# Kernel optimization log

Measured on AMD Instinct MI355X. Metric: run time of the kernel, lower is better.

## Reference

```python
import jax, jax.numpy as jnp
import numpy as np

N = 50000
E = 800000
D = 128


def _gcn_layer(x, row, col, ew, W, b, n):
    # PyG GCNConv (normalize=True, add_self_loops=True):
    # self-loops were already appended to row/col/ew by the caller.
    deg = jax.ops.segment_sum(ew, col, num_segments=n)          # [N]
    dis = jnp.where(deg > 0, jax.lax.rsqrt(jnp.maximum(deg, 1e-12)), 0.0)
    norm = dis[row] * ew * dis[col]                              # [E+N]
    h = x @ W                                                    # [N, D]
    msg = h[row] * norm[:, None]                                 # [E+N, D] gather-scale
    out = jax.ops.segment_sum(msg, col, num_segments=n)          # scatter-add
    return out + b


def setup_inputs() -> dict:
    key = jax.random.key(0)
    k1, k2, k3, k4, k5 = jax.random.split(key, 5)
    x = jax.random.normal(k1, (N, D), dtype=jnp.float32)
    edge_index = jax.random.randint(k2, (2, E), 0, N, dtype=jnp.int64)
    edge_weight = jax.random.uniform(k3, (E,), dtype=jnp.float32)
    s = 1.0 / np.sqrt(D)
    W1 = jax.random.uniform(k4, (D, D), minval=-s, maxval=s, dtype=jnp.float32)
    b1 = jnp.zeros((D,), dtype=jnp.float32)
    W2 = jax.random.uniform(k5, (D, D), minval=-s, maxval=s, dtype=jnp.float32)
    b2 = jnp.zeros((D,), dtype=jnp.float32)
    return {"x": x, "edge_index": edge_index, "edge_weight": edge_weight,
            "W1": W1, "b1": b1, "W2": W2, "b2": b2}


def reference(x, edge_index, edge_weight, W1, b1, W2, b2):
    n = x.shape[0]
    loop = jnp.arange(n, dtype=edge_index.dtype)
    row = jnp.concatenate([edge_index[0], loop])
    col = jnp.concatenate([edge_index[1], loop])
    ew = jnp.concatenate([edge_weight, jnp.ones((n,), dtype=edge_weight.dtype)])
    h = _gcn_layer(x, row, col, ew, W1, b1, n)
    h = jax.nn.relu(h)
    # F.dropout(training=self.training): identity in eval mode
    out = _gcn_layer(h, row, col, ew, W2, b2, n)
    return out
```

## Files before the change

### kernel.cpp

```cpp
#include <hip/hip_runtime.h>

#define NN 50000
#define NE 800000
#define DD 128

#define FIX_SCALE 16777216.0f
#define LOW40 ((1ULL << 40) - 1)
#define NWELEM 16384
#define GEMM_GRID ((NN + 127) / 128)

#define SHIFT2 7
#define BWID 128
#define NBUCK ((NN + BWID - 1) / BWID)
#define CAP2 2560
#define NB1 500
#define EPB (NE / NB1)
#define EQ4 (EPB / 4)
#define NBK_PAD 392
#define HCAP 1536

typedef __attribute__((ext_vector_type(8))) short short8;
typedef __attribute__((ext_vector_type(4))) float floatx4;
typedef __attribute__((ext_vector_type(2))) _Float16 half2v;
typedef __attribute__((ext_vector_type(8))) _Float16 half8;


__device__ __forceinline__ void split_trunc(float x, short& hi, short& lo) {
    unsigned uh = __float_as_uint(x) >> 16;
    hi = (short)uh;
    float r = x - __uint_as_float(uh << 16);
    lo = (short)(__float_as_uint(r) >> 16);
}


__global__ __launch_bounds__(256) void init_hist(const int* __restrict__ col,
                                                 unsigned* __restrict__ hist,
                                                 const float* __restrict__ W1, const float* __restrict__ W2,
                                                 unsigned short* __restrict__ w1hi, unsigned short* __restrict__ w1lo,
                                                 unsigned short* __restrict__ w2hi, unsigned short* __restrict__ w2lo) {
    if (blockIdx.x < NB1) {
        __shared__ unsigned h[NBUCK];
        for (int k = threadIdx.x; k < NBUCK; k += 256) h[k] = 0u;
        __syncthreads();
        const int4* c4p = (const int4*)(col + blockIdx.x * EPB);
#pragma unroll
        for (int it = 0; it < 2; it++) {
            int q = it * 256 + (int)threadIdx.x;
            if (q < EQ4) {
                int4 c4 = c4p[q];
                atomicAdd(&h[c4.x >> SHIFT2], 1u);
                atomicAdd(&h[c4.y >> SHIFT2], 1u);
                atomicAdd(&h[c4.z >> SHIFT2], 1u);
                atomicAdd(&h[c4.w >> SHIFT2], 1u);
            }
        }
        __syncthreads();
        unsigned* hb = hist + (size_t)blockIdx.x * NBK_PAD;
        for (int k = threadIdx.x; k < NBUCK; k += 256) hb[k] = h[k];
    } else {
        int u = (blockIdx.x - NB1) * 256 + threadIdx.x;
        int which = u >> 14;
        int idx = u & (NWELEM - 1);
        int k = idx >> 7, n = idx & 127;
        const float* W = which ? W2 : W1;
        unsigned short* whi = which ? w2hi : w1hi;
        unsigned short* wlo = which ? w2lo : w1lo;
        short h, l;
        split_trunc(W[idx], h, l);
        whi[n * DD + k] = (unsigned short)h;
        wlo[n * DD + k] = (unsigned short)l;
    }
}


__global__ __launch_bounds__(512) void bucket_prefix(const unsigned* __restrict__ hist,
                                                     unsigned* __restrict__ offs_t,
                                                     unsigned* __restrict__ bcur) {
    __shared__ unsigned sa[512], sb[512];
    int k = blockIdx.x;
    int t = threadIdx.x;
    unsigned v = (t < NB1) ? hist[(size_t)t * NBK_PAD + k] : 0u;
    sa[t] = v;
    __syncthreads();
    unsigned* src = sa;
    unsigned* dst = sb;
    for (int d = 1; d < 512; d <<= 1) {
        unsigned x = src[t] + (t >= d ? src[t - d] : 0u);
        dst[t] = x;
        __syncthreads();
        unsigned* tmp = src; src = dst; dst = tmp;
    }
    unsigned inc = src[t];
    if (t < NB1) offs_t[(size_t)t * NBK_PAD + k] = inc - v;
    if (t == 511) bcur[k] = inc;
}


template <bool RELU, bool SCALE, typename InT>
__device__ __forceinline__ void gemm_core(int bid, const InT* __restrict__ in,
                                          const unsigned short* __restrict__ whi,
                                          const unsigned short* __restrict__ wlo,
                                          const float* __restrict__ dis,
                                          _Float16* __restrict__ out) {
    int lane = threadIdx.x & 63;
    int wid = threadIdx.x >> 6;
    int cg = wid & 1;
    int rg = wid >> 1;
    int l16 = lane & 15;
    int quad = lane >> 4;
    int koff_base = quad * 8;

    short8 bhi[4][4], blo[4][4];
#pragma unroll
    for (int t = 0; t < 4; t++) {
        int n = cg * 64 + t * 16 + l16;
#pragma unroll
        for (int ks = 0; ks < 4; ks++) {
            int koff = ks * 32 + koff_base;
            bhi[t][ks] = *(const short8*)(whi + n * DD + koff);
            blo[t][ks] = *(const short8*)(wlo + n * DD + koff);
        }
    }

#pragma unroll
    for (int chunk = 0; chunk < 4; chunk++) {
        int base = bid * 128 + chunk * 32 + rg * 16;
        int m = base + l16;
        int mld = (m < NN) ? m : 0;
        const InT* xr = in + (size_t)mld * DD;

        short8 ahi[4], alo[4];
#pragma unroll
        for (int ks = 0; ks < 4; ks++) {
            int koff = ks * 32 + koff_base;
            float v[8];
            if constexpr (sizeof(InT) == 4) {
                float4 a0 = *(const float4*)(xr + koff);
                float4 a1 = *(const float4*)(xr + koff + 4);
                v[0] = a0.x; v[1] = a0.y; v[2] = a0.z; v[3] = a0.w;
                v[4] = a1.x; v[5] = a1.y; v[6] = a1.z; v[7] = a1.w;
            } else {
                half8 a = *(const half8*)(xr + koff);
#pragma unroll
                for (int j = 0; j < 8; j++) v[j] = (float)a[j];
            }
#pragma unroll
            for (int j = 0; j < 8; j++) {
                float xv = RELU ? fmaxf(v[j], 0.0f) : v[j];
                short h, l;
                split_trunc(xv, h, l);
                ahi[ks][j] = h;
                alo[ks][j] = l;
            }
        }

        floatx4 acc[4];
#pragma unroll
        for (int t = 0; t < 4; t++) acc[t] = (floatx4)(0.0f);

#pragma unroll
        for (int ks = 0; ks < 4; ks++) {
#pragma unroll
            for (int t = 0; t < 4; t++) {
                acc[t] = __builtin_amdgcn_mfma_f32_16x16x32_bf16(ahi[ks], bhi[t][ks], acc[t], 0, 0, 0);
                acc[t] = __builtin_amdgcn_mfma_f32_16x16x32_bf16(alo[ks], bhi[t][ks], acc[t], 0, 0, 0);
                acc[t] = __builtin_amdgcn_mfma_f32_16x16x32_bf16(ahi[ks], blo[t][ks], acc[t], 0, 0, 0);
            }
        }

#pragma unroll
        for (int r = 0; r < 4; r++) {
            int rowm = base + quad * 4 + r;
            if (rowm < NN) {
                float dsc = SCALE ? dis[rowm] : 1.0f;
                _Float16* o = out + (size_t)rowm * DD + cg * 64 + l16;
#pragma unroll
                for (int t = 0; t < 4; t++) o[t * 16] = (_Float16)(acc[t][r] * dsc);
            }
        }
    }
}


__device__ __forceinline__ void scatter_core(int bid, const int* __restrict__ row,
                                             const int* __restrict__ col,
                                             const float* __restrict__ ew,
                                             const unsigned* __restrict__ offs_t,
                                             uint2* __restrict__ staged) {
    __shared__ unsigned base1[NBUCK];
    __shared__ unsigned cnt1[NBUCK];

    const unsigned* ob = offs_t + (size_t)bid * NBK_PAD;
    for (int k = threadIdx.x; k < NBUCK; k += 256) {
        base1[k] = (unsigned)k * CAP2 + ob[k];
        cnt1[k] = 0u;
    }
    __syncthreads();

    int e0 = bid * EPB;
    const int4* c4p = (const int4*)(col + e0);
    const int4* r4p = (const int4*)(row + e0);
    const float4* w4p = (const float4*)(ew + e0);

#pragma unroll
    for (int it = 0; it < 2; it++) {
        int q = it * 256 + (int)threadIdx.x;
        if (q < EQ4) {
            int4 c4 = c4p[q];
            int4 r4 = r4p[q];
            float4 w4 = w4p[q];
            int cc[4] = {c4.x, c4.y, c4.z, c4.w};
            int rr[4] = {r4.x, r4.y, r4.z, r4.w};
            float wv[4] = {w4.x, w4.y, w4.z, w4.w};
#pragma unroll
            for (int j = 0; j < 4; j++) {
                int bk = cc[j] >> SHIFT2;
                unsigned r = base1[bk] + atomicAdd(&cnt1[bk], 1u);
                unsigned lim = (unsigned)bk * CAP2 + (CAP2 - 1);
                if (r > lim) r = lim;
                uint2 p;
                p.x = (unsigned)rr[j] | ((unsigned)(cc[j] & (BWID - 1)) << 16);
                p.y = __float_as_uint(wv[j]);
                staged[r] = p;
            }
        }
    }
}


__global__ __launch_bounds__(256) void gemm1_scatter(const float* __restrict__ x,
                                                     const unsigned short* __restrict__ w1hi,
                                                     const unsigned short* __restrict__ w1lo,
                                                     _Float16* __restrict__ g,
                                                     const int* __restrict__ row,
                                                     const int* __restrict__ col,
                                                     const float* __restrict__ ew,
                                                     const unsigned* __restrict__ offs_t,
                                                     uint2* __restrict__ staged) {
    if (blockIdx.x < NB1) {
        scatter_core(blockIdx.x, row, col, ew, offs_t, staged);
    } else {
        gemm_core<false, false, float>(blockIdx.x - NB1, x, w1hi, w1lo, nullptr, g);
    }
}

__global__ __launch_bounds__(256, 2) void gemm2(const _Float16* __restrict__ in,
                                                const unsigned short* __restrict__ whi,
                                                const unsigned short* __restrict__ wlo,
                                                const float* __restrict__ dis,
                                                _Float16* __restrict__ out) {
    gemm_core<true, true, _Float16>(blockIdx.x, in, whi, wlo, dis, out);
}


__global__ __launch_bounds__(512) void bucket_sortdis(const unsigned* __restrict__ bcur,
                                                      const uint2* __restrict__ staged,
                                                      uint2* __restrict__ sorted,
                                                      unsigned* __restrict__ offcnt,
                                                      float* __restrict__ dis,
                                                      _Float16* __restrict__ g) {
    __shared__ uint2 sRAW[CAP2];
    __shared__ uint2 sED[CAP2];
    __shared__ unsigned long long wcnt[BWID];
    __shared__ unsigned sc[BWID];
    __shared__ unsigned offs[BWID];
    __shared__ unsigned cur[BWID];
    __shared__ float disS[BWID];

    int b = blockIdx.x;
    int node0 = b << SHIFT2;
    int nn = min(BWID, NN - node0);
    int t = threadIdx.x;

    if (t < BWID) { wcnt[t] = 0ULL; cur[t] = 0u; }
    __syncthreads();

    int m = min((int)bcur[b], CAP2);
    const uint2* st = staged + (size_t)b * CAP2;

    for (int j = t; j < m; j += 512) {
        uint2 p = st[j];
        sRAW[j] = p;
        int ln = p.x >> 16;
        float w = __uint_as_float(p.y);
        unsigned q = (unsigned)(w * FIX_SCALE + 0.5f);
        atomicAdd(&wcnt[ln], (1ULL << 40) | (unsigned long long)q);
    }
    __syncthreads();

    if (t < BWID) sc[t] = (unsigned)(wcnt[t] >> 40);
    __syncthreads();
    for (int d = 1; d < BWID; d <<= 1) {
        unsigned v = 0;
        if (t < BWID) { v = sc[t]; if (t >= d) v += sc[t - d]; }
        __syncthreads();
        if (t < BWID) sc[t] = v;
        __syncthreads();
    }
    if (t < BWID) {
        unsigned long long cv = wcnt[t];
        unsigned c = (unsigned)(cv >> 40);
        unsigned off = sc[t] - c;
        offs[t] = off;
        if (t < (unsigned)nn) {
            int i = node0 + t;
            float deg = 1.0f + (float)(cv & LOW40) * (1.0f / FIX_SCALE);
            float d = rsqrtf(deg);
            disS[t] = d;
            dis[i] = d;
            offcnt[i] = (off << 16) | c;
        }
    }
    __syncthreads();

    for (int j = t; j < m; j += 512) {
        uint2 p = sRAW[j];
        int ln = p.x >> 16;
        unsigned r = offs[ln] + atomicAdd(&cur[ln], 1u);
        uint2 q;
        q.x = (p.x & 0xFFFFu) << 7;
        q.y = p.y;
        sED[r] = q;
    }
    __syncthreads();
    uint2* dst = sorted + (size_t)b * CAP2;
    int m2 = (m + 1) >> 1;
    for (int j = t; j < m2; j += 512) ((uint4*)dst)[j] = ((const uint4*)sED)[j];

    half8* gb = (half8*)(g + (size_t)node0 * DD);
    for (int idx = t; idx < nn * 16; idx += 512) {
        float d = disS[idx >> 4];
        half8 hv = gb[idx];
#pragma unroll
        for (int jj = 0; jj < 8; jj++) hv[jj] = (_Float16)((float)hv[jj] * d);
        gb[idx] = hv;
    }
}


template <typename OutT>
__global__ __launch_bounds__(512) void agg_gather(const uint2* __restrict__ sorted,
                                                  const unsigned* __restrict__ offcnt,
                                                  const _Float16* __restrict__ g,
                                                  const float* __restrict__ dis,
                                                  const float* __restrict__ bias,
                                                  OutT* __restrict__ out) {
    __shared__ uint2 sED[HCAP];

    int hb = blockIdx.x;
    int b = hb >> 1;
    int half = hb & 1;
    int node0 = (b << SHIFT2) + half * 64;
    int nloc = min(64, NN - node0);

    unsigned ocf = offcnt[node0];
    unsigned ocl = offcnt[node0 + nloc - 1];
    int first = (int)(ocf >> 16);
    int end = (int)(ocl >> 16) + (int)(ocl & 0xFFFFu);
    int mloc = min(end - first, HCAP);

    const uint2* st = sorted + (size_t)b * CAP2 + first;
    for (int j = threadIdx.x; j < mloc; j += 512) sED[j] = st[j];
    __syncthreads();

    int wid = threadIdx.x >> 6;
    int lane = threadIdx.x & 63;

    for (int ln = wid; ln < nloc; ln += 8) {
        int i = node0 + ln;
        unsigned oc = offcnt[i];
        int s0 = (int)(oc >> 16) - first;
        int e0 = min(s0 + (int)(oc & 0xFFFFu), mloc);
        float a0 = 0.0f, a1 = 0.0f;
        int j = s0;
        for (; j + 7 < e0; j += 8) {
            uint2 p0 = sED[j],     p1 = sED[j + 1], p2 = sED[j + 2], p3 = sED[j + 3];
            uint2 p4 = sED[j + 4], p5 = sED[j + 5], p6 = sED[j + 6], p7 = sED[j + 7];
            half2v v0 = *(const half2v*)(g + p0.x + 2 * lane);
            half2v v1 = *(const half2v*)(g + p1.x + 2 * lane);
            half2v v2 = *(const half2v*)(g + p2.x + 2 * lane);
            half2v v3 = *(const half2v*)(g + p3.x + 2 * lane);
            half2v v4 = *(const half2v*)(g + p4.x + 2 * lane);
            half2v v5 = *(const half2v*)(g + p5.x + 2 * lane);
            half2v v6 = *(const half2v*)(g + p6.x + 2 * lane);
            half2v v7 = *(const half2v*)(g + p7.x + 2 * lane);
            float w0 = __uint_as_float(p0.y), w1 = __uint_as_float(p1.y);
            float w2 = __uint_as_float(p2.y), w3 = __uint_as_float(p3.y);
            float w4 = __uint_as_float(p4.y), w5 = __uint_as_float(p5.y);
            float w6 = __uint_as_float(p6.y), w7 = __uint_as_float(p7.y);
            a0 = fmaf(w0, (float)v0.x, a0); a1 = fmaf(w0, (float)v0.y, a1);
            a0 = fmaf(w1, (float)v1.x, a0); a1 = fmaf(w1, (float)v1.y, a1);
            a0 = fmaf(w2, (float)v2.x, a0); a1 = fmaf(w2, (float)v2.y, a1);
            a0 = fmaf(w3, (float)v3.x, a0); a1 = fmaf(w3, (float)v3.y, a1);
            a0 = fmaf(w4, (float)v4.x, a0); a1 = fmaf(w4, (float)v4.y, a1);
            a0 = fmaf(w5, (float)v5.x, a0); a1 = fmaf(w5, (float)v5.y, a1);
            a0 = fmaf(w6, (float)v6.x, a0); a1 = fmaf(w6, (float)v6.y, a1);
            a0 = fmaf(w7, (float)v7.x, a0); a1 = fmaf(w7, (float)v7.y, a1);
        }
        for (; j + 3 < e0; j += 4) {
            uint2 p0 = sED[j], p1 = sED[j + 1], p2 = sED[j + 2], p3 = sED[j + 3];
            half2v v0 = *(const half2v*)(g + p0.x + 2 * lane);
            half2v v1 = *(const half2v*)(g + p1.x + 2 * lane);
            half2v v2 = *(const half2v*)(g + p2.x + 2 * lane);
            half2v v3 = *(const half2v*)(g + p3.x + 2 * lane);
            float w0 = __uint_as_float(p0.y), w1 = __uint_as_float(p1.y);
            float w2 = __uint_as_float(p2.y), w3 = __uint_as_float(p3.y);
            a0 = fmaf(w0, (float)v0.x, a0); a1 = fmaf(w0, (float)v0.y, a1);
            a0 = fmaf(w1, (float)v1.x, a0); a1 = fmaf(w1, (float)v1.y, a1);
            a0 = fmaf(w2, (float)v2.x, a0); a1 = fmaf(w2, (float)v2.y, a1);
            a0 = fmaf(w3, (float)v3.x, a0); a1 = fmaf(w3, (float)v3.y, a1);
        }
        for (; j < e0; ++j) {
            uint2 p0 = sED[j];
            half2v v0 = *(const half2v*)(g + p0.x + 2 * lane);
            float w0 = __uint_as_float(p0.y);
            a0 = fmaf(w0, (float)v0.x, a0); a1 = fmaf(w0, (float)v0.y, a1);
        }
        float d = dis[i];
        half2v gs = *(const half2v*)(g + (size_t)i * DD + 2 * lane);
        float2 bb = *(const float2*)(bias + 2 * lane);
        float o0 = bb.x + d * (a0 + (float)gs.x);
        float o1 = bb.y + d * (a1 + (float)gs.y);
        if constexpr (sizeof(OutT) == 2) {
            half2v o; o.x = (_Float16)o0; o.y = (_Float16)o1;
            *(half2v*)(out + (size_t)i * DD + 2 * lane) = o;
        } else {
            float2 o; o.x = o0; o.y = o1;
            *(float2*)(out + (size_t)i * DD + 2 * lane) = o;
        }
    }
}


extern "C" void kernel_launch(void* const* d_in, const int* in_sizes, int n_in,
                              void* d_out, int out_size, void* d_ws, size_t ws_size,
                              hipStream_t stream) {
    const float* x  = (const float*)d_in[0];
    const int*   ei = (const int*)d_in[1];
    const float* ew = (const float*)d_in[2];
    const float* W1 = (const float*)d_in[3];
    const float* b1 = (const float*)d_in[4];
    const float* W2 = (const float*)d_in[5];
    const float* b2 = (const float*)d_in[6];
    float* out = (float*)d_out;

    float* ws      = (float*)d_ws;
    float* dis     = ws;
    unsigned* bcur = (unsigned*)(ws + 50000);
    unsigned* offcnt = (unsigned*)(ws + 100000);
    unsigned* hist = (unsigned*)(ws + 150000);
    unsigned* offs_t = (unsigned*)(ws + 400000);
    uint2* staged  = (uint2*)(ws + 900000);
    uint2* sorted  = (uint2*)(ws + 3000000);
    _Float16* gbuf = (_Float16*)(ws + 7300000);
    unsigned short* wt1hi = (unsigned short*)(ws + 10500000);
    unsigned short* wt1lo = (unsigned short*)(ws + 10508192);
    unsigned short* wt2hi = (unsigned short*)(ws + 10516384);
    unsigned short* wt2lo = (unsigned short*)(ws + 10524576);
    _Float16* out1 = (_Float16*)(ws + 10532768);

    const int* rowi = ei;
    const int* coli = ei + NE;

    init_hist<<<NB1 + (2 * NWELEM) / 256, 256, 0, stream>>>(
        coli, hist, W1, W2, wt1hi, wt1lo, wt2hi, wt2lo);

    bucket_prefix<<<NBUCK, 512, 0, stream>>>(hist, offs_t, bcur);

    gemm1_scatter<<<NB1 + GEMM_GRID, 256, 0, stream>>>(
        x, wt1hi, wt1lo, gbuf, rowi, coli, ew, offs_t, staged);

    bucket_sortdis<<<NBUCK, 512, 0, stream>>>(bcur, staged, sorted, offcnt, dis, gbuf);

    const int agg_grid = 2 * NBUCK;

    agg_gather<_Float16><<<agg_grid, 512, 0, stream>>>(sorted, offcnt, gbuf, dis, b1, out1);

    gemm2<<<GEMM_GRID, 256, 0, stream>>>(out1, wt2hi, wt2lo, dis, gbuf);

    agg_gather<float><<<agg_grid, 512, 0, stream>>>(sorted, offcnt, gbuf, dis, b2, out);
}
```

Before: 214.0 us.

## Replace histogram+prefix kernels with in-block counting and global atomic bucket reservation

Removes the separate per-block histogram kernel and the per-bucket prefix-scan kernel. Each scatter block now counts its bucket occupancy in shared memory and reserves space with one global atomicAdd per bucket, and bcur is zeroed in a merged init kernel. The aggregation kernel is also re-gridded into smaller blocks (16 nodes, 256 threads, smaller shared staging) for more parallelism, and its 4-wide tail loop is dropped. The edge order within a bucket is now nondeterministic, and the smaller shared cap could truncate edges when 16 nodes have many edges.

```diff
diff --git a/kernel.cpp b/kernel.cpp
--- a/kernel.cpp
+++ b/kernel.cpp
@@ -16,8 +16,7 @@
 #define NB1 500
 #define EPB (NE / NB1)
 #define EQ4 (EPB / 4)
-#define NBK_PAD 392
-#define HCAP 1536
+#define SCAP 640
 
 typedef __attribute__((ext_vector_type(8))) short short8;
 typedef __attribute__((ext_vector_type(4))) float floatx4;
@@ -33,32 +32,14 @@
 }
 
 
-__global__ __launch_bounds__(256) void init_hist(const int* __restrict__ col,
-                                                 unsigned* __restrict__ hist,
-                                                 const float* __restrict__ W1, const float* __restrict__ W2,
-                                                 unsigned short* __restrict__ w1hi, unsigned short* __restrict__ w1lo,
-                                                 unsigned short* __restrict__ w2hi, unsigned short* __restrict__ w2lo) {
-    if (blockIdx.x < NB1) {
-        __shared__ unsigned h[NBUCK];
-        for (int k = threadIdx.x; k < NBUCK; k += 256) h[k] = 0u;
-        __syncthreads();
-        const int4* c4p = (const int4*)(col + blockIdx.x * EPB);
-#pragma unroll
-        for (int it = 0; it < 2; it++) {
-            int q = it * 256 + (int)threadIdx.x;
-            if (q < EQ4) {
-                int4 c4 = c4p[q];
-                atomicAdd(&h[c4.x >> SHIFT2], 1u);
-                atomicAdd(&h[c4.y >> SHIFT2], 1u);
-                atomicAdd(&h[c4.z >> SHIFT2], 1u);
-                atomicAdd(&h[c4.w >> SHIFT2], 1u);
-            }
-        }
-        __syncthreads();
-        unsigned* hb = hist + (size_t)blockIdx.x * NBK_PAD;
-        for (int k = threadIdx.x; k < NBUCK; k += 256) hb[k] = h[k];
-    } else {
-        int u = (blockIdx.x - NB1) * 256 + threadIdx.x;
+__global__ __launch_bounds__(256) void init_ws(unsigned* __restrict__ bcur,
+                                               const float* __restrict__ W1, const float* __restrict__ W2,
+                                               unsigned short* __restrict__ w1hi, unsigned short* __restrict__ w1lo,
+                                               unsigned short* __restrict__ w2hi, unsigned short* __restrict__ w2lo) {
+    int t = blockIdx.x * blockDim.x + threadIdx.x;
+    if (t < NBUCK) bcur[t] = 0u;
+    int u = t - 512;
+    if (u >= 0 && u < 2 * NWELEM) {
         int which = u >> 14;
         int idx = u & (NWELEM - 1);
         int k = idx >> 7, n = idx & 127;
@@ -70,29 +51,6 @@
         whi[n * DD + k] = (unsigned short)h;
         wlo[n * DD + k] = (unsigned short)l;
     }
-}
-
-
-__global__ __launch_bounds__(512) void bucket_prefix(const unsigned* __restrict__ hist,
-                                                     unsigned* __restrict__ offs_t,
-                                                     unsigned* __restrict__ bcur) {
-    __shared__ unsigned sa[512], sb[512];
-    int k = blockIdx.x;
-    int t = threadIdx.x;
-    unsigned v = (t < NB1) ? hist[(size_t)t * NBK_PAD + k] : 0u;
-    sa[t] = v;
-    __syncthreads();
-    unsigned* src = sa;
-    unsigned* dst = sb;
-    for (int d = 1; d < 512; d <<= 1) {
-        unsigned x = src[t] + (t >= d ? src[t - d] : 0u);
-        dst[t] = x;
-        __syncthreads();
-        unsigned* tmp = src; src = dst; dst = tmp;
-    }
-    unsigned inc = src[t];
-    if (t < NB1) offs_t[(size_t)t * NBK_PAD + k] = inc - v;
-    if (t == 511) bcur[k] = inc;
 }
 
 
@@ -185,22 +143,38 @@
 __device__ __forceinline__ void scatter_core(int bid, const int* __restrict__ row,
                                              const int* __restrict__ col,
                                              const float* __restrict__ ew,
-                                             const unsigned* __restrict__ offs_t,
+                                             unsigned* __restrict__ bcur,
                                              uint2* __restrict__ staged) {
+    __shared__ unsigned cnt1[NBUCK];
     __shared__ unsigned base1[NBUCK];
-    __shared__ unsigned cnt1[NBUCK];
-
-    const unsigned* ob = offs_t + (size_t)bid * NBK_PAD;
-    for (int k = threadIdx.x; k < NBUCK; k += 256) {
-        base1[k] = (unsigned)k * CAP2 + ob[k];
-        cnt1[k] = 0u;
-    }
+
+    for (int k = threadIdx.x; k < NBUCK; k += 256) cnt1[k] = 0u;
     __syncthreads();
 
     int e0 = bid * EPB;
     const int4* c4p = (const int4*)(col + e0);
     const int4* r4p = (const int4*)(row + e0);
     const float4* w4p = (const float4*)(ew + e0);
+
+#pragma unroll
+    for (int it = 0; it < 2; it++) {
+        int q = it * 256 + (int)threadIdx.x;
+        if (q < EQ4) {
+            int4 c4 = c4p[q];
+            atomicAdd(&cnt1[c4.x >> SHIFT2], 1u);
+            atomicAdd(&cnt1[c4.y >> SHIFT2], 1u);
+            atomicAdd(&cnt1[c4.z >> SHIFT2], 1u);
+            atomicAdd(&cnt1[c4.w >> SHIFT2], 1u);
+        }
+    }
+    __syncthreads();
+
+    for (int k = threadIdx.x; k < NBUCK; k += 256) {
+        unsigned n = cnt1[k];
+        base1[k] = (unsigned)k * CAP2 + (n ? atomicAdd(&bcur[k], n) : 0u);
+        cnt1[k] = 0u;
+    }
+    __syncthreads();
 
 #pragma unroll
     for (int it = 0; it < 2; it++) {
@@ -235,10 +209,10 @@
                                                      const int* __restrict__ row,
                                                      const int* __restrict__ col,
                                                      const float* __restrict__ ew,
-                                                     const unsigned* __restrict__ offs_t,
+                                                     unsigned* __restrict__ bcur,
                                                      uint2* __restrict__ staged) {
     if (blockIdx.x < NB1) {
-        scatter_core(blockIdx.x, row, col, ew, offs_t, staged);
+        scatter_core(blockIdx.x, row, col, ew, bcur, staged);
     } else {
         gemm_core<false, false, float>(blockIdx.x - NB1, x, w1hi, w1lo, nullptr, g);
     }
@@ -339,34 +313,35 @@
 
 
 template <typename OutT>
-__global__ __launch_bounds__(512) void agg_gather(const uint2* __restrict__ sorted,
+__global__ __launch_bounds__(256) void agg_gather(const uint2* __restrict__ sorted,
                                                   const unsigned* __restrict__ offcnt,
                                                   const _Float16* __restrict__ g,
                                                   const float* __restrict__ dis,
                                                   const float* __restrict__ bias,
                                                   OutT* __restrict__ out) {
-    __shared__ uint2 sED[HCAP];
-
-    int hb = blockIdx.x;
-    int b = hb >> 1;
-    int half = hb & 1;
-    int node0 = (b << SHIFT2) + half * 64;
-    int nloc = min(64, NN - node0);
+    __shared__ uint2 sED[SCAP];
+
+    int gb = blockIdx.x;
+    int b = gb >> 3;
+    int sub = gb & 7;
+    int node0 = (b << SHIFT2) + sub * 16;
+    if (node0 >= NN) return;
+    int nloc = min(16, NN - node0);
 
     unsigned ocf = offcnt[node0];
     unsigned ocl = offcnt[node0 + nloc - 1];
     int first = (int)(ocf >> 16);
     int end = (int)(ocl >> 16) + (int)(ocl & 0xFFFFu);
-    int mloc = min(end - first, HCAP);
+    int mloc = min(end - first, SCAP);
 
     const uint2* st = sorted + (size_t)b * CAP2 + first;
-    for (int j = threadIdx.x; j < mloc; j += 512) sED[j] = st[j];
+    for (int j = threadIdx.x; j < mloc; j += 256) sED[j] = st[j];
     __syncthreads();
 
     int wid = threadIdx.x >> 6;
     int lane = threadIdx.x & 63;
 
-    for (int ln = wid; ln < nloc; ln += 8) {
+    for (int ln = wid; ln < nloc; ln += 4) {
         int i = node0 + ln;
         unsigned oc = offcnt[i];
         int s0 = (int)(oc >> 16) - first;
@@ -397,19 +372,6 @@
             a0 = fmaf(w6, (float)v6.x, a0); a1 = fmaf(w6, (float)v6.y, a1);
             a0 = fmaf(w7, (float)v7.x, a0); a1 = fmaf(w7, (float)v7.y, a1);
         }
-        for (; j + 3 < e0; j += 4) {
-            uint2 p0 = sED[j], p1 = sED[j + 1], p2 = sED[j + 2], p3 = sED[j + 3];
-            half2v v0 = *(const half2v*)(g + p0.x + 2 * lane);
-            half2v v1 = *(const half2v*)(g + p1.x + 2 * lane);
-            half2v v2 = *(const half2v*)(g + p2.x + 2 * lane);
-            half2v v3 = *(const half2v*)(g + p3.x + 2 * lane);
-            float w0 = __uint_as_float(p0.y), w1 = __uint_as_float(p1.y);
-            float w2 = __uint_as_float(p2.y), w3 = __uint_as_float(p3.y);
-            a0 = fmaf(w0, (float)v0.x, a0); a1 = fmaf(w0, (float)v0.y, a1);
-            a0 = fmaf(w1, (float)v1.x, a0); a1 = fmaf(w1, (float)v1.y, a1);
-            a0 = fmaf(w2, (float)v2.x, a0); a1 = fmaf(w2, (float)v2.y, a1);
-            a0 = fmaf(w3, (float)v3.x, a0); a1 = fmaf(w3, (float)v3.y, a1);
-        }
         for (; j < e0; ++j) {
             uint2 p0 = sED[j];
             half2v v0 = *(const half2v*)(g + p0.x + 2 * lane);
@@ -448,8 +410,6 @@
     float* dis     = ws;
     unsigned* bcur = (unsigned*)(ws + 50000);
     unsigned* offcnt = (unsigned*)(ws + 100000);
-    unsigned* hist = (unsigned*)(ws + 150000);
-    unsigned* offs_t = (unsigned*)(ws + 400000);
     uint2* staged  = (uint2*)(ws + 900000);
     uint2* sorted  = (uint2*)(ws + 3000000);
     _Float16* gbuf = (_Float16*)(ws + 7300000);
@@ -462,21 +422,19 @@
     const int* rowi = ei;
     const int* coli = ei + NE;
 
-    init_hist<<<NB1 + (2 * NWELEM) / 256, 256, 0, stream>>>(
-        coli, hist, W1, W2, wt1hi, wt1lo, wt2hi, wt2lo);
-
-    bucket_prefix<<<NBUCK, 512, 0, stream>>>(hist, offs_t, bcur);
+    init_ws<<<(512 + 2 * NWELEM + 255) / 256, 256, 0, stream>>>(
+        bcur, W1, W2, wt1hi, wt1lo, wt2hi, wt2lo);
 
     gemm1_scatter<<<NB1 + GEMM_GRID, 256, 0, stream>>>(
-        x, wt1hi, wt1lo, gbuf, rowi, coli, ew, offs_t, staged);
+        x, wt1hi, wt1lo, gbuf, rowi, coli, ew, bcur, staged);
 
     bucket_sortdis<<<NBUCK, 512, 0, stream>>>(bcur, staged, sorted, offcnt, dis, gbuf);
 
-    const int agg_grid = 2 * NBUCK;
-
-    agg_gather<_Float16><<<agg_grid, 512, 0, stream>>>(sorted, offcnt, gbuf, dis, b1, out1);
+    const int agg_grid = 8 * NBUCK;
+
+    agg_gather<_Float16><<<agg_grid, 256, 0, stream>>>(sorted, offcnt, gbuf, dis, b1, out1);
 
     gemm2<<<GEMM_GRID, 256, 0, stream>>>(out1, wt2hi, wt2lo, dis, gbuf);
 
-    agg_gather<float><<<agg_grid, 512, 0, stream>>>(sorted, offcnt, gbuf, dis, b2, out);
-}
+    agg_gather<float><<<agg_grid, 256, 0, stream>>>(sorted, offcnt, gbuf, dis, b2, out);
+}
```

Result: slower. 222.5 us (+4.0%).

## Move layer-1 source normalization into gather and double scatter block count

Applied to the files above, without the earlier changes.

The in-place pass in bucket_sortdis that scaled every gathered feature row by dis is removed. Layer-1 aggregation now multiplies each edge weight by dis[src] inside the gather loop instead. The histogram and scatter stage also moves from 500 to 1000 blocks with one quad per thread, and the prefix scan is widened to 1024 threads to match. The 4-wide remainder loop in the gather is dropped. This saves a full read-modify-write of the feature matrix, at the cost of an extra random dis load per edge and a longer prefix scan.

```diff
diff --git a/kernel.cpp b/kernel.cpp
--- a/kernel.cpp
+++ b/kernel.cpp
@@ -13,7 +13,7 @@
 #define BWID 128
 #define NBUCK ((NN + BWID - 1) / BWID)
 #define CAP2 2560
-#define NB1 500
+#define NB1 1000
 #define EPB (NE / NB1)
 #define EQ4 (EPB / 4)
 #define NBK_PAD 392
@@ -43,16 +43,13 @@
         for (int k = threadIdx.x; k < NBUCK; k += 256) h[k] = 0u;
         __syncthreads();
         const int4* c4p = (const int4*)(col + blockIdx.x * EPB);
-#pragma unroll
-        for (int it = 0; it < 2; it++) {
-            int q = it * 256 + (int)threadIdx.x;
-            if (q < EQ4) {
-                int4 c4 = c4p[q];
-                atomicAdd(&h[c4.x >> SHIFT2], 1u);
-                atomicAdd(&h[c4.y >> SHIFT2], 1u);
-                atomicAdd(&h[c4.z >> SHIFT2], 1u);
-                atomicAdd(&h[c4.w >> SHIFT2], 1u);
-            }
+        int q = (int)threadIdx.x;
+        if (q < EQ4) {
+            int4 c4 = c4p[q];
+            atomicAdd(&h[c4.x >> SHIFT2], 1u);
+            atomicAdd(&h[c4.y >> SHIFT2], 1u);
+            atomicAdd(&h[c4.z >> SHIFT2], 1u);
+            atomicAdd(&h[c4.w >> SHIFT2], 1u);
         }
         __syncthreads();
         unsigned* hb = hist + (size_t)blockIdx.x * NBK_PAD;
@@ -73,10 +70,10 @@
 }
 
 
-__global__ __launch_bounds__(512) void bucket_prefix(const unsigned* __restrict__ hist,
-                                                     unsigned* __restrict__ offs_t,
-                                                     unsigned* __restrict__ bcur) {
-    __shared__ unsigned sa[512], sb[512];
+__global__ __launch_bounds__(1024) void bucket_prefix(const unsigned* __restrict__ hist,
+                                                      unsigned* __restrict__ offs_t,
+                                                      unsigned* __restrict__ bcur) {
+    __shared__ unsigned sa[1024], sb[1024];
     int k = blockIdx.x;
     int t = threadIdx.x;
     unsigned v = (t < NB1) ? hist[(size_t)t * NBK_PAD + k] : 0u;
@@ -84,7 +81,7 @@
     __syncthreads();
     unsigned* src = sa;
     unsigned* dst = sb;
-    for (int d = 1; d < 512; d <<= 1) {
+    for (int d = 1; d < 1024; d <<= 1) {
         unsigned x = src[t] + (t >= d ? src[t - d] : 0u);
         dst[t] = x;
         __syncthreads();
@@ -92,7 +89,7 @@
     }
     unsigned inc = src[t];
     if (t < NB1) offs_t[(size_t)t * NBK_PAD + k] = inc - v;
-    if (t == 511) bcur[k] = inc;
+    if (t == 1023) bcur[k] = inc;
 }
 
 
@@ -202,27 +199,24 @@
     const int4* r4p = (const int4*)(row + e0);
     const float4* w4p = (const float4*)(ew + e0);
 
-#pragma unroll
-    for (int it = 0; it < 2; it++) {
-        int q = it * 256 + (int)threadIdx.x;
-        if (q < EQ4) {
-            int4 c4 = c4p[q];
-            int4 r4 = r4p[q];
-            float4 w4 = w4p[q];
-            int cc[4] = {c4.x, c4.y, c4.z, c4.w};
-            int rr[4] = {r4.x, r4.y, r4.z, r4.w};
-            float wv[4] = {w4.x, w4.y, w4.z, w4.w};
-#pragma unroll
-            for (int j = 0; j < 4; j++) {
-                int bk = cc[j] >> SHIFT2;
-                unsigned r = base1[bk] + atomicAdd(&cnt1[bk], 1u);
-                unsigned lim = (unsigned)bk * CAP2 + (CAP2 - 1);
-                if (r > lim) r = lim;
-                uint2 p;
-                p.x = (unsigned)rr[j] | ((unsigned)(cc[j] & (BWID - 1)) << 16);
-                p.y = __float_as_uint(wv[j]);
-                staged[r] = p;
-            }
+    int q = (int)threadIdx.x;
+    if (q < EQ4) {
+        int4 c4 = c4p[q];
+        int4 r4 = r4p[q];
+        float4 w4 = w4p[q];
+        int cc[4] = {c4.x, c4.y, c4.z, c4.w};
+        int rr[4] = {r4.x, r4.y, r4.z, r4.w};
+        float wv[4] = {w4.x, w4.y, w4.z, w4.w};
+#pragma unroll
+        for (int j = 0; j < 4; j++) {
+            int bk = cc[j] >> SHIFT2;
+            unsigned r = base1[bk] + atomicAdd(&cnt1[bk], 1u);
+            unsigned lim = (unsigned)bk * CAP2 + (CAP2 - 1);
+            if (r > lim) r = lim;
+            uint2 p;
+            p.x = (unsigned)rr[j] | ((unsigned)(cc[j] & (BWID - 1)) << 16);
+            p.y = __float_as_uint(wv[j]);
+            staged[r] = p;
         }
     }
 }
@@ -257,15 +251,13 @@
                                                       const uint2* __restrict__ staged,
                                                       uint2* __restrict__ sorted,
                                                       unsigned* __restrict__ offcnt,
-                                                      float* __restrict__ dis,
-                                                      _Float16* __restrict__ g) {
+                                                      float* __restrict__ dis) {
     __shared__ uint2 sRAW[CAP2];
     __shared__ uint2 sED[CAP2];
     __shared__ unsigned long long wcnt[BWID];
     __shared__ unsigned sc[BWID];
     __shared__ unsigned offs[BWID];
     __shared__ unsigned cur[BWID];
-    __shared__ float disS[BWID];
 
     int b = blockIdx.x;
     int node0 = b << SHIFT2;
@@ -305,9 +297,7 @@
         if (t < (unsigned)nn) {
             int i = node0 + t;
             float deg = 1.0f + (float)(cv & LOW40) * (1.0f / FIX_SCALE);
-            float d = rsqrtf(deg);
-            disS[t] = d;
-            dis[i] = d;
+            dis[i] = rsqrtf(deg);
             offcnt[i] = (off << 16) | c;
         }
     }
@@ -326,19 +316,10 @@
     uint2* dst = sorted + (size_t)b * CAP2;
     int m2 = (m + 1) >> 1;
     for (int j = t; j < m2; j += 512) ((uint4*)dst)[j] = ((const uint4*)sED)[j];
-
-    half8* gb = (half8*)(g + (size_t)node0 * DD);
-    for (int idx = t; idx < nn * 16; idx += 512) {
-        float d = disS[idx >> 4];
-        half8 hv = gb[idx];
-#pragma unroll
-        for (int jj = 0; jj < 8; jj++) hv[jj] = (_Float16)((float)hv[jj] * d);
-        gb[idx] = hv;
-    }
-}
-
-
-template <typename OutT>
+}
+
+
+template <bool EDGE_DIS, typename OutT>
 __global__ __launch_bounds__(512) void agg_gather(const uint2* __restrict__ sorted,
                                                   const unsigned* __restrict__ offcnt,
                                                   const _Float16* __restrict__ g,
@@ -388,6 +369,12 @@
             float w2 = __uint_as_float(p2.y), w3 = __uint_as_float(p3.y);
             float w4 = __uint_as_float(p4.y), w5 = __uint_as_float(p5.y);
             float w6 = __uint_as_float(p6.y), w7 = __uint_as_float(p7.y);
+            if constexpr (EDGE_DIS) {
+                w0 *= dis[p0.x >> 7]; w1 *= dis[p1.x >> 7];
+                w2 *= dis[p2.x >> 7]; w3 *= dis[p3.x >> 7];
+                w4 *= dis[p4.x >> 7]; w5 *= dis[p5.x >> 7];
+                w6 *= dis[p6.x >> 7]; w7 *= dis[p7.x >> 7];
+            }
             a0 = fmaf(w0, (float)v0.x, a0); a1 = fmaf(w0, (float)v0.y, a1);
             a0 = fmaf(w1, (float)v1.x, a0); a1 = fmaf(w1, (float)v1.y, a1);
             a0 = fmaf(w2, (float)v2.x, a0); a1 = fmaf(w2, (float)v2.y, a1);
@@ -397,30 +384,20 @@
             a0 = fmaf(w6, (float)v6.x, a0); a1 = fmaf(w6, (float)v6.y, a1);
             a0 = fmaf(w7, (float)v7.x, a0); a1 = fmaf(w7, (float)v7.y, a1);
         }
-        for (; j + 3 < e0; j += 4) {
-            uint2 p0 = sED[j], p1 = sED[j + 1], p2 = sED[j + 2], p3 = sED[j + 3];
-            half2v v0 = *(const half2v*)(g + p0.x + 2 * lane);
-            half2v v1 = *(const half2v*)(g + p1.x + 2 * lane);
-            half2v v2 = *(const half2v*)(g + p2.x + 2 * lane);
-            half2v v3 = *(const half2v*)(g + p3.x + 2 * lane);
-            float w0 = __uint_as_float(p0.y), w1 = __uint_as_float(p1.y);
-            float w2 = __uint_as_float(p2.y), w3 = __uint_as_float(p3.y);
-            a0 = fmaf(w0, (float)v0.x, a0); a1 = fmaf(w0, (float)v0.y, a1);
-            a0 = fmaf(w1, (float)v1.x, a0); a1 = fmaf(w1, (float)v1.y, a1);
-            a0 = fmaf(w2, (float)v2.x, a0); a1 = fmaf(w2, (float)v2.y, a1);
-            a0 = fmaf(w3, (float)v3.x, a0); a1 = fmaf(w3, (float)v3.y, a1);
-        }
         for (; j < e0; ++j) {
             uint2 p0 = sED[j];
             half2v v0 = *(const half2v*)(g + p0.x + 2 * lane);
             float w0 = __uint_as_float(p0.y);
+            if constexpr (EDGE_DIS) w0 *= dis[p0.x >> 7];
             a0 = fmaf(w0, (float)v0.x, a0); a1 = fmaf(w0, (float)v0.y, a1);
         }
         float d = dis[i];
         half2v gs = *(const half2v*)(g + (size_t)i * DD + 2 * lane);
         float2 bb = *(const float2*)(bias + 2 * lane);
-        float o0 = bb.x + d * (a0 + (float)gs.x);
-        float o1 = bb.y + d * (a1 + (float)gs.y);
+        float s0v = EDGE_DIS ? d * (float)gs.x : (float)gs.x;
+        float s1v = EDGE_DIS ? d * (float)gs.y : (float)gs.y;
+        float o0 = bb.x + d * (a0 + s0v);
+        float o1 = bb.y + d * (a1 + s1v);
         if constexpr (sizeof(OutT) == 2) {
             half2v o; o.x = (_Float16)o0; o.y = (_Float16)o1;
             *(half2v*)(out + (size_t)i * DD + 2 * lane) = o;
@@ -449,9 +426,9 @@
     unsigned* bcur = (unsigned*)(ws + 50000);
     unsigned* offcnt = (unsigned*)(ws + 100000);
     unsigned* hist = (unsigned*)(ws + 150000);
-    unsigned* offs_t = (unsigned*)(ws + 400000);
-    uint2* staged  = (uint2*)(ws + 900000);
-    uint2* sorted  = (uint2*)(ws + 3000000);
+    unsigned* offs_t = (unsigned*)(ws + 550000);
+    uint2* staged  = (uint2*)(ws + 1000000);
+    uint2* sorted  = (uint2*)(ws + 3100000);
     _Float16* gbuf = (_Float16*)(ws + 7300000);
     unsigned short* wt1hi = (unsigned short*)(ws + 10500000);
     unsigned short* wt1lo = (unsigned short*)(ws + 10508192);
@@ -465,18 +442,18 @@
     init_hist<<<NB1 + (2 * NWELEM) / 256, 256, 0, stream>>>(
         coli, hist, W1, W2, wt1hi, wt1lo, wt2hi, wt2lo);
 
-    bucket_prefix<<<NBUCK, 512, 0, stream>>>(hist, offs_t, bcur);
+    bucket_prefix<<<NBUCK, 1024, 0, stream>>>(hist, offs_t, bcur);
 
     gemm1_scatter<<<NB1 + GEMM_GRID, 256, 0, stream>>>(
         x, wt1hi, wt1lo, gbuf, rowi, coli, ew, offs_t, staged);
 
-    bucket_sortdis<<<NBUCK, 512, 0, stream>>>(bcur, staged, sorted, offcnt, dis, gbuf);
+    bucket_sortdis<<<NBUCK, 512, 0, stream>>>(bcur, staged, sorted, offcnt, dis);
 
     const int agg_grid = 2 * NBUCK;
 
-    agg_gather<_Float16><<<agg_grid, 512, 0, stream>>>(sorted, offcnt, gbuf, dis, b1, out1);
+    agg_gather<true, _Float16><<<agg_grid, 512, 0, stream>>>(sorted, offcnt, gbuf, dis, b1, out1);
 
     gemm2<<<GEMM_GRID, 256, 0, stream>>>(out1, wt2hi, wt2lo, dis, gbuf);
 
-    agg_gather<float><<<agg_grid, 512, 0, stream>>>(sorted, offcnt, gbuf, dis, b2, out);
-}
+    agg_gather<false, float><<<agg_grid, 512, 0, stream>>>(sorted, offcnt, gbuf, dis, b2, out);
+}
```

Result: slower. 221.2 us (+3.4%).
